# Performance work log

Hardware: AMD Instinct MI355X
Metric: run time of the kernel (lower is better)

Reference implementation:

```python
import jax, jax.numpy as jnp
import numpy as np

B, N, F_IN = 64, 128, 128
H, MSG, L = 512, 512, 4
N_STEPS = 4
TARGET = 12
HIDDEN = (128, 256, 128)


def _mlp_params(key, n_in, n_out):
    dims = (n_in,) + HIDDEN + (n_out,)
    ps = []
    for i in range(len(dims) - 1):
        key, k1, k2 = jax.random.split(key, 3)
        s = 1.0 / np.sqrt(dims[i]).astype(np.float32)
        ps.append(jax.random.uniform(k1, (dims[i + 1], dims[i]), minval=-s, maxval=s, dtype=jnp.float32))
        ps.append(jax.random.uniform(k2, (dims[i + 1],), minval=-s, maxval=s, dtype=jnp.float32))
    return ps


def setup_inputs():
    key = jax.random.key(0)
    ks = jax.random.split(key, 10)
    g = (jax.random.uniform(ks[0], (B, N, N)) < 0.15).astype(jnp.float32)
    e = jax.random.randint(ks[1], (B, N, N), 0, L + 1).astype(jnp.float32) * g
    h_in = jax.random.normal(ks[2], (B, N, F_IN), dtype=jnp.float32)
    # trailing nodes are 'virtual' (zero features -> masked out by the model)
    node_on = (jnp.arange(N) < 112).astype(jnp.float32)
    h_in = h_in * node_on[None, :, None]
    g = g * node_on[None, :, None] * node_on[None, None, :]
    e = e * node_on[None, :, None] * node_on[None, None, :]
    A = jax.random.normal(ks[3], (L, H, MSG), dtype=jnp.float32)  # per-edge-label message matrices
    s = 1.0 / np.sqrt(H).astype(np.float32)
    gru_Wih = jax.random.uniform(ks[4], (3 * H, MSG), minval=-s, maxval=s, dtype=jnp.float32)
    gru_Whh = jax.random.uniform(ks[5], (3 * H, H), minval=-s, maxval=s, dtype=jnp.float32)
    gru_bih = jax.random.uniform(ks[6], (3 * H,), minval=-s, maxval=s, dtype=jnp.float32)
    gru_bhh = jax.random.uniform(ks[7], (3 * H,), minval=-s, maxval=s, dtype=jnp.float32)
    r1 = _mlp_params(ks[8], 2 * H, TARGET)
    r2 = _mlp_params(ks[9], H, TARGET)
    inp = dict(g=g, h_in=h_in, e=e, A=A, gru_Wih=gru_Wih, gru_Whh=gru_Whh,
               gru_bih=gru_bih, gru_bhh=gru_bhh)
    for i in range(4):
        inp['r1_W%d' % i], inp['r1_b%d' % i] = r1[2 * i], r1[2 * i + 1]
        inp['r2_W%d' % i], inp['r2_b%d' % i] = r2[2 * i], r2[2 * i + 1]
    return inp


def _mlp(x, Ws, bs):
    for W, b in zip(Ws[:-1], bs[:-1]):
        x = jax.nn.relu(x @ W.T + b)
    return x @ Ws[-1].T + bs[-1]


def _forward(g, h_in, e, A, gru_Wih, gru_Whh, gru_bih, gru_bhh, r1_Ws, r1_bs, r2_Ws, r2_bs):
    Bq, Nq, F = h_in.shape
    Lq, Hq, Mq = A.shape
    # zero-pad node features up to hidden size
    h0 = jnp.concatenate([h_in, jnp.zeros((Bq, Nq, Hq - F), h_in.dtype)], axis=-1)  # [B,N,H]
    node_mask = (jnp.sum(jnp.abs(h_in), axis=-1) > 0).astype(h_in.dtype)  # [B,N]
    labels = jnp.arange(1, Lq + 1, dtype=e.dtype)
    e_oh = (e[..., None] == labels).astype(h_in.dtype)  # [B,N,N,L] edge-label one-hot
    h = h0
    for _ in range(N_STEPS):
        # per-label projected states, then edge-conditioned masked-sum aggregation
        hproj = jnp.einsum('bwh,lhm->blwm', h, A)  # [B,L,N,MSG]
        m = jnp.einsum('bvwl,blwm,bvw->bvm', e_oh, hproj, g)  # [B,N,MSG]
        # one GRU step per node (vectorized), torch nn.GRU gate ordering r,z,n
        gi = m @ gru_Wih.T + gru_bih
        gh = h @ gru_Whh.T + gru_bhh
        i_r, i_z, i_n = jnp.split(gi, 3, axis=-1)
        h_r, h_z, h_n = jnp.split(gh, 3, axis=-1)
        r = jax.nn.sigmoid(i_r + h_r)
        z = jax.nn.sigmoid(i_z + h_z)
        n = jnp.tanh(i_n + r * h_n)
        h = ((1.0 - z) * n + z * h) * node_mask[..., None]
    # GGNN gated readout over nodes, masking virtual nodes
    gate = jax.nn.sigmoid(_mlp(jnp.concatenate([h, h0], axis=-1), r1_Ws, r1_bs))
    val = _mlp(h, r2_Ws, r2_bs)
    read_mask = (jnp.sum(h0, axis=-1) != 0).astype(h.dtype)  # [B,N]
    return jnp.sum(gate * val * read_mask[..., None], axis=1)  # [B,TARGET]


def reference(g, h_in, e, A, gru_Wih, gru_Whh, gru_bih, gru_bhh,
              r1_W0, r1_b0, r1_W1, r1_b1, r1_W2, r1_b2, r1_W3, r1_b3,
              r2_W0, r2_b0, r2_W1, r2_b1, r2_W2, r2_b2, r2_W3, r2_b3):
    return _forward(g, h_in, e, A, gru_Wih, gru_Whh, gru_bih, gru_bhh,
                    [r1_W0, r1_W1, r1_W2, r1_W3], [r1_b0, r1_b1, r1_b2, r1_b3],
                    [r2_W0, r2_W1, r2_W2, r2_W3], [r2_b0, r2_b1, r2_b2, r2_b3])
```

## Files before the change

kernel.cpp:

```cpp
#include <hip/hip_runtime.h>
#include <math.h>

#define B_     64
#define N_     128
#define FIN_   128
#define H_     512
#define MSG_   512
#define L_     4
#define NSTEPS_ 4
#define TGT_   12
#define ROWS_  (B_*N_)

typedef _Float16 f16;
typedef __attribute__((ext_vector_type(8))) _Float16 half8;
typedef __attribute__((ext_vector_type(4))) float f32x4;

__device__ inline void gload16(const void* g, void* l) {
    __builtin_amdgcn_global_load_lds((const __attribute__((address_space(1))) void*)g,
                                     (__attribute__((address_space(3))) void*)l,
                                     16, 0, 0);
}

__device__ inline void split_write(float v, f16* ph, f16* pl) {
    f16 hi = (f16)v;
    *ph = hi;
    *pl = (f16)(v - (float)hi);
}

__global__ void k_init(const float* __restrict__ h_in,
                       f16* __restrict__ hbh, f16* __restrict__ hbl,
                       float* __restrict__ nmask, float* __restrict__ rmask) {
    int bn = blockIdx.x;
    int t  = threadIdx.x;
    const float* src = h_in + (size_t)bn * FIN_;
    float v  = src[t];
    float sa = fabsf(v), ss = v;
    #pragma unroll
    for (int o = 32; o > 0; o >>= 1) {
        sa += __shfl_down(sa, o);
        ss += __shfl_down(ss, o);
    }
    __shared__ float wa[2], wsum[2];
    int wid = t >> 6, lane = t & 63;
    if (lane == 0) { wa[wid] = sa; wsum[wid] = ss; }
    __syncthreads();
    if (t == 0) {
        float ta = wa[0] + wa[1], ts = wsum[0] + wsum[1];
        nmask[bn] = (ta > 0.f) ? 1.f : 0.f;
        rmask[bn] = (ts != 0.f) ? 1.f : 0.f;
    }
    f16* bh = hbh + (size_t)bn * 1024;
    f16* bl = hbl + (size_t)bn * 1024;
    #pragma unroll
    for (int r = 0; r < 4; r++) {
        int j = t + r * 128;
        float val = (j < FIN_) ? src[j] : 0.f;
        f16 hi = (f16)val, lo = (f16)(val - (float)hi);
        bh[j] = hi; bl[j] = lo;
        bh[512 + j] = hi; bl[512 + j] = lo;
    }
}

__global__ void k_mkmask(const float* __restrict__ g, const float* __restrict__ e,
                         f16* __restrict__ Mm) {
    long idx = (long)blockIdx.x * 256 + threadIdx.x;
    if (idx >= (long)ROWS_ * 512) return;
    int w = idx & 127;
    int l = (idx >> 7) & 3;
    long bv = idx >> 9;
    float gv = g[bv * N_ + w];
    float ev = e[bv * N_ + w];
    Mm[idx] = (f16)((gv != 0.f && (int)ev == l + 1) ? 1.f : 0.f);
}

struct WSet {
    const float* s[10];
    f16* d[10];
    int nc[10];
    int ncp[10];
    int kk[10];
};
__global__ void k_convWs(WSet ws) {
    int ti = blockIdx.y;
    long idx = (long)blockIdx.x * 256 + threadIdx.x;
    int K = ws.kk[ti];
    long tot = (long)ws.ncp[ti] * K;
    if (idx >= tot) return;
    long n = idx / K;
    ws.d[ti][idx] = (f16)((n < ws.nc[ti]) ? ws.s[ti][idx] : 0.f);
}

__global__ void k_convA(const float* __restrict__ A, f16* __restrict__ ATh,
                        f16* __restrict__ ATl) {
    long idx = (long)blockIdx.x * 256 + threadIdx.x;
    long n = idx >> 11, k = idx & 2047;
    float v = A[k * 512 + n];
    f16 hi = (f16)v;
    ATh[idx] = hi;
    ATl[idx] = (f16)(v - (float)hi);
}

__global__ __launch_bounds__(256, 3)
void k_proj(const f16* __restrict__ ATh, const f16* __restrict__ ATl,
            const f16* __restrict__ hb, f16* __restrict__ oh, f16* __restrict__ ol)
{
    __shared__ __align__(16) f16 As[2][2][4][128][8];
    __shared__ __align__(16) f16 Bs[2][4][128][8];
    const int tid = threadIdx.x;
    const int l = tid & 63, w = tid >> 6;
    const int wr = w >> 1, wc = w & 1;
    const int lz = blockIdx.z;
    const long m0 = (long)blockIdx.x * 128;
    const long n0 = (long)blockIdx.y * 128;

    f32x4 acc[4][4];
    #pragma unroll
    for (int i = 0; i < 4; i++)
        #pragma unroll
        for (int j = 0; j < 4; j++)
            acc[i][j] = (f32x4){0.f, 0.f, 0.f, 0.f};

    const int nt = 512 >> 5;

    auto stage = [&](int buf, int t) {
        long k0 = (long)t << 5;
        #pragma unroll
        for (int i = 0; i < 4; ++i) {
            int la = tid + i * 256;
            int row = la & 127, c = (la >> 7) & 3, pl = la >> 9;
            const f16* Xp = pl ? ATl : ATh;
            gload16(Xp + (m0 + row) * 2048 + lz * 512 + k0 + c * 8,
                    (f16*)As[buf] + (size_t)la * 8);
        }
        #pragma unroll
        for (int i = 0; i < 2; ++i) {
            int la = tid + i * 256;
            int col = la & 127, c = la >> 7;
            gload16(hb + (n0 + col) * 1024 + k0 + c * 8,
                    (f16*)Bs[buf] + (size_t)la * 8);
        }
    };

    stage(0, 0);
    for (int t = 0; t < nt; ++t) {
        int cur = t & 1;
        __syncthreads();
        if (t + 1 < nt) stage(cur ^ 1, t + 1);
        const int g = l >> 4, idx = l & 15;
        half8 bf[4];
        #pragma unroll
        for (int ct = 0; ct < 4; ++ct)
            bf[ct] = *(const half8*)&Bs[cur][g][wc * 64 + ct * 16 + idx][0];
        #pragma unroll
        for (int rt = 0; rt < 4; ++rt) {
            half8 ah = *(const half8*)&As[cur][0][g][wr * 64 + rt * 16 + idx][0];
            half8 al = *(const half8*)&As[cur][1][g][wr * 64 + rt * 16 + idx][0];
            #pragma unroll
            for (int ct = 0; ct < 4; ++ct) {
                acc[rt][ct] = __builtin_amdgcn_mfma_f32_16x16x32_f16(ah, bf[ct], acc[rt][ct], 0, 0, 0);
                acc[rt][ct] = __builtin_amdgcn_mfma_f32_16x16x32_f16(al, bf[ct], acc[rt][ct], 0, 0, 0);
            }
        }
    }

    #pragma unroll
    for (int rt = 0; rt < 4; ++rt)
        #pragma unroll
        for (int ct = 0; ct < 4; ++ct) {
            long col = n0 + wc * 64 + ct * 16 + (l & 15);
            long bb = col >> 7, ww = col & 127;
            #pragma unroll
            for (int j = 0; j < 4; ++j) {
                long row = m0 + wr * 64 + rt * 16 + (l >> 4) * 4 + j;
                size_t o = ((size_t)(bb * 512 + row)) * 512 + lz * 128 + ww;
                split_write(acc[rt][ct][j], oh + o, ol + o);
            }
        }
}

__global__ __launch_bounds__(256, 3)
void k_aggm(const f16* __restrict__ Mm, const f16* __restrict__ ph,
            const f16* __restrict__ pl_, f16* __restrict__ mh, f16* __restrict__ ml)
{
    __shared__ __align__(16) f16 As[2][4][128][8];
    __shared__ __align__(16) f16 Bs[2][2][4][128][8];
    const int tid = threadIdx.x;
    const int l = tid & 63, w = tid >> 6;
    const int wr = w >> 1, wc = w & 1;
    const long b  = blockIdx.y;
    const long n0 = (long)blockIdx.x * 128;
    const f16* Xb = Mm  + (size_t)b * 128 * 512;
    const f16* W0 = ph  + (size_t)b * 512 * 512;
    const f16* W1 = pl_ + (size_t)b * 512 * 512;

    f32x4 acc[4][4];
    #pragma unroll
    for (int i = 0; i < 4; i++)
        #pragma unroll
        for (int j = 0; j < 4; j++)
            acc[i][j] = (f32x4){0.f, 0.f, 0.f, 0.f};

    const int nt = 512 >> 5;

    auto stage = [&](int buf, int t) {
        long k0 = (long)t << 5;
        #pragma unroll
        for (int i = 0; i < 2; ++i) {
            int la = tid + i * 256;
            int row = la & 127, c = la >> 7;
            gload16(Xb + row * 512 + k0 + c * 8, (f16*)As[buf] + (size_t)la * 8);
        }
        #pragma unroll
        for (int i = 0; i < 4; ++i) {
            int la = tid + i * 256;
            int col = la & 127, c = (la >> 7) & 3, pl = la >> 9;
            gload16((pl ? W1 : W0) + (n0 + col) * 512 + k0 + c * 8,
                    (f16*)Bs[buf][pl] + (size_t)(la & 511) * 8);
        }
    };

    stage(0, 0);
    for (int t = 0; t < nt; ++t) {
        int cur = t & 1;
        __syncthreads();
        if (t + 1 < nt) stage(cur ^ 1, t + 1);
        const int g = l >> 4, idx = l & 15;
        half8 bfh[4], bfl[4];
        #pragma unroll
        for (int ct = 0; ct < 4; ++ct) {
            bfh[ct] = *(const half8*)&Bs[cur][0][g][wc * 64 + ct * 16 + idx][0];
            bfl[ct] = *(const half8*)&Bs[cur][1][g][wc * 64 + ct * 16 + idx][0];
        }
        #pragma unroll
        for (int rt = 0; rt < 4; ++rt) {
            half8 af = *(const half8*)&As[cur][g][wr * 64 + rt * 16 + idx][0];
            #pragma unroll
            for (int ct = 0; ct < 4; ++ct) {
                acc[rt][ct] = __builtin_amdgcn_mfma_f32_16x16x32_f16(af, bfh[ct], acc[rt][ct], 0, 0, 0);
                acc[rt][ct] = __builtin_amdgcn_mfma_f32_16x16x32_f16(af, bfl[ct], acc[rt][ct], 0, 0, 0);
            }
        }
    }

    #pragma unroll
    for (int rt = 0; rt < 4; ++rt)
        #pragma unroll
        for (int ct = 0; ct < 4; ++ct) {
            long col = n0 + wc * 64 + ct * 16 + (l & 15);
            #pragma unroll
            for (int j = 0; j < 4; ++j) {
                long row = wr * 64 + rt * 16 + (l >> 4) * 4 + j;
                size_t o = ((size_t)b * 128 + row) * 512 + col;
                split_write(acc[rt][ct][j], mh + o, ml + o);
            }
        }
}

__global__ __launch_bounds__(256, 2)
void k_gruG(const f16* __restrict__ mh, const f16* __restrict__ ml,
            const f16* __restrict__ Wih,
            const f16* __restrict__ hih, const f16* __restrict__ hil,
            const f16* __restrict__ Whh,
            const float* __restrict__ bih, const float* __restrict__ bhh,
            f16* __restrict__ hoh, f16* __restrict__ hol,
            const float* __restrict__ nmask)
{
    __shared__ __align__(16) f16 As[2][2][4][128][8];
    __shared__ __align__(16) f16 Bs[2][4][192][8];
    const int tid = threadIdx.x;
    const int l = tid & 63, w = tid >> 6;
    const int wr = w >> 1, wc = w & 1;
    const long m0 = (long)blockIdx.x * 128;
    const int  c0 = blockIdx.y * 64;

    f32x4 rz[2][4][2], ni[4][2], nh[4][2];
    #pragma unroll
    for (int rt = 0; rt < 4; ++rt)
        #pragma unroll
        for (int ct = 0; ct < 2; ++ct) {
            rz[0][rt][ct] = (f32x4){0.f, 0.f, 0.f, 0.f};
            rz[1][rt][ct] = (f32x4){0.f, 0.f, 0.f, 0.f};
            ni[rt][ct]    = (f32x4){0.f, 0.f, 0.f, 0.f};
            nh[rt][ct]    = (f32x4){0.f, 0.f, 0.f, 0.f};
        }

    auto stageB = [&](int buf, int t, const f16* W) {
        long k0 = (long)t << 5;
        #pragma unroll
        for (int i = 0; i < 3; ++i) {
            int la = tid + i * 256;
            int g = la / 192, cc = la - g * 192;
            int col = (cc >> 6) * 512 + c0 + (cc & 63);
            gload16(W + (size_t)col * 512 + k0 + g * 8,
                    (f16*)Bs[buf] + ((size_t)g * 192 + cc) * 8);
        }
    };
    auto stage1 = [&](int buf, int t) {
        long k0 = (long)t << 5;
        #pragma unroll
        for (int i = 0; i < 4; ++i) {
            int la = tid + i * 256;
            int pl = la >> 9, g = (la >> 7) & 3, row = la & 127;
            const f16* Xp = pl ? ml : mh;
            gload16(Xp + (m0 + row) * 512 + k0 + g * 8,
                    (f16*)As[buf][pl] + (size_t)(la & 511) * 8);
        }
        stageB(buf, t, Wih);
    };
    auto stage2 = [&](int buf, int t) {
        long k0 = (long)t << 5;
        #pragma unroll
        for (int i = 0; i < 2; ++i) {
            int la = tid + i * 256;
            int g = la >> 7, row = la & 127;
            gload16(hih + (m0 + row) * 1024 + k0 + g * 8,
                    (f16*)As[buf][0] + (size_t)la * 8);
        }
        stageB(buf, t, Whh);
    };

    const int g = l >> 4, idx = l & 15;

    stage1(0, 0);
    for (int t = 0; t < 16; ++t) {
        int cur = t & 1;
        __syncthreads();
        if (t + 1 < 16) stage1(cur ^ 1, t + 1);
        half8 bf[6];
        #pragma unroll
        for (int gc = 0; gc < 6; ++gc)
            bf[gc] = *(const half8*)&Bs[cur][g][(gc >> 1) * 64 + wc * 32 + (gc & 1) * 16 + idx][0];
        #pragma unroll
        for (int rt = 0; rt < 4; ++rt) {
            half8 ah = *(const half8*)&As[cur][0][g][wr * 64 + rt * 16 + idx][0];
            half8 al = *(const half8*)&As[cur][1][g][wr * 64 + rt * 16 + idx][0];
            #pragma unroll
            for (int ct = 0; ct < 2; ++ct) {
                rz[0][rt][ct] = __builtin_amdgcn_mfma_f32_16x16x32_f16(ah, bf[ct],     rz[0][rt][ct], 0, 0, 0);
                rz[0][rt][ct] = __builtin_amdgcn_mfma_f32_16x16x32_f16(al, bf[ct],     rz[0][rt][ct], 0, 0, 0);
                rz[1][rt][ct] = __builtin_amdgcn_mfma_f32_16x16x32_f16(ah, bf[2 + ct], rz[1][rt][ct], 0, 0, 0);
                rz[1][rt][ct] = __builtin_amdgcn_mfma_f32_16x16x32_f16(al, bf[2 + ct], rz[1][rt][ct], 0, 0, 0);
                ni[rt][ct]    = __builtin_amdgcn_mfma_f32_16x16x32_f16(ah, bf[4 + ct], ni[rt][ct],    0, 0, 0);
                ni[rt][ct]    = __builtin_amdgcn_mfma_f32_16x16x32_f16(al, bf[4 + ct], ni[rt][ct],    0, 0, 0);
            }
        }
    }

    stage2(0, 0);
    for (int t = 0; t < 16; ++t) {
        int cur = t & 1;
        __syncthreads();
        if (t + 1 < 16) stage2(cur ^ 1, t + 1);
        half8 bf[6];
        #pragma unroll
        for (int gc = 0; gc < 6; ++gc)
            bf[gc] = *(const half8*)&Bs[cur][g][(gc >> 1) * 64 + wc * 32 + (gc & 1) * 16 + idx][0];
        #pragma unroll
        for (int rt = 0; rt < 4; ++rt) {
            half8 ah = *(const half8*)&As[cur][0][g][wr * 64 + rt * 16 + idx][0];
            #pragma unroll
            for (int ct = 0; ct < 2; ++ct) {
                rz[0][rt][ct] = __builtin_amdgcn_mfma_f32_16x16x32_f16(ah, bf[ct],     rz[0][rt][ct], 0, 0, 0);
                rz[1][rt][ct] = __builtin_amdgcn_mfma_f32_16x16x32_f16(ah, bf[2 + ct], rz[1][rt][ct], 0, 0, 0);
                nh[rt][ct]    = __builtin_amdgcn_mfma_f32_16x16x32_f16(ah, bf[4 + ct], nh[rt][ct],    0, 0, 0);
            }
        }
    }

    #pragma unroll
    for (int rt = 0; rt < 4; ++rt)
        #pragma unroll
        for (int ct = 0; ct < 2; ++ct) {
            int c = c0 + wc * 32 + ct * 16 + idx;
            float br = bih[c]        + bhh[c];
            float bz = bih[512 + c]  + bhh[512 + c];
            float bni = bih[1024 + c];
            float bnh = bhh[1024 + c];
            #pragma unroll
            for (int j = 0; j < 4; ++j) {
                long row = m0 + wr * 64 + rt * 16 + g * 4 + j;
                float r = 1.f / (1.f + expf(-(rz[0][rt][ct][j] + br)));
                float z = 1.f / (1.f + expf(-(rz[1][rt][ct][j] + bz)));
                float n = tanhf(ni[rt][ct][j] + bni + r * (nh[rt][ct][j] + bnh));
                size_t o = (size_t)row * 1024 + c;
                float h_old = (float)hih[o] + (float)hil[o];
                float out = ((1.f - z) * n + z * h_old) * nmask[row];
                split_write(out, hoh + o, hol + o);
            }
        }
}

template<int OUT>
__global__ __launch_bounds__(256, 4)
void k_mfma1(const f16* __restrict__ Xh, int ldx,
             const f16* __restrict__ Wh, int ldw, const float* __restrict__ bias,
             float* __restrict__ Cf, f16* __restrict__ Ch,
             int ldc, int ncmax, int K)
{
    __shared__ __align__(16) f16 As[2][4][128][8];
    __shared__ __align__(16) f16 Bs[2][4][128][8];
    const int tid = threadIdx.x;
    const int l = tid & 63, w = tid >> 6;
    const int wr = w >> 1, wc = w & 1;
    const long m0 = (long)blockIdx.x * 128;
    const long n0 = (long)blockIdx.y * 128;

    f32x4 acc[4][4];
    #pragma unroll
    for (int i = 0; i < 4; i++)
        #pragma unroll
        for (int j = 0; j < 4; j++)
            acc[i][j] = (f32x4){0.f, 0.f, 0.f, 0.f};

    const int nt = K >> 5;

    auto stage = [&](int buf, int t) {
        long k0 = (long)t << 5;
        #pragma unroll
        for (int i = 0; i < 2; ++i) {
            int la = tid + i * 256;
            int row = la & 127, c = la >> 7;
            gload16(Xh + (m0 + row) * ldx + k0 + c * 8,
                    (f16*)As[buf] + (size_t)la * 8);
        }
        #pragma unroll
        for (int i = 0; i < 2; ++i) {
            int la = tid + i * 256;
            int col = la & 127, c = la >> 7;
            gload16(Wh + (n0 + col) * ldw + k0 + c * 8,
                    (f16*)Bs[buf] + (size_t)la * 8);
        }
    };

    stage(0, 0);
    for (int t = 0; t < nt; ++t) {
        int cur = t & 1;
        __syncthreads();
        if (t + 1 < nt) stage(cur ^ 1, t + 1);
        const int g = l >> 4, idx = l & 15;
        half8 bf[4];
        #pragma unroll
        for (int ct = 0; ct < 4; ++ct)
            bf[ct] = *(const half8*)&Bs[cur][g][wc * 64 + ct * 16 + idx][0];
        #pragma unroll
        for (int rt = 0; rt < 4; ++rt) {
            half8 ah = *(const half8*)&As[cur][g][wr * 64 + rt * 16 + idx][0];
            #pragma unroll
            for (int ct = 0; ct < 4; ++ct)
                acc[rt][ct] = __builtin_amdgcn_mfma_f32_16x16x32_f16(ah, bf[ct], acc[rt][ct], 0, 0, 0);
        }
    }

    #pragma unroll
    for (int rt = 0; rt < 4; ++rt)
        #pragma unroll
        for (int ct = 0; ct < 4; ++ct) {
            long col = n0 + wc * 64 + ct * 16 + (l & 15);
            if (col < ncmax) {
                float bv = bias ? bias[col] : 0.f;
                #pragma unroll
                for (int j = 0; j < 4; ++j) {
                    long row = m0 + wr * 64 + rt * 16 + (l >> 4) * 4 + j;
                    float v = acc[rt][ct][j] + bv;
                    if (OUT == 0) {
                        Cf[row * ldc + col] = v;
                    } else {
                        Ch[row * ldc + col] = (f16)fmaxf(v, 0.f);
                    }
                }
            }
        }
}

__global__ void k_readout(const float* __restrict__ gp, const float* __restrict__ vp,
                          const float* __restrict__ rmask, float* __restrict__ out) {
    int b = blockIdx.x;
    int t = threadIdx.x;
    float a[TGT_];
    const float* gr = gp + ((size_t)b * N_ + t) * TGT_;
    const float* vr = vp + ((size_t)b * N_ + t) * TGT_;
    float mk = rmask[b * N_ + t];
    #pragma unroll
    for (int j = 0; j < TGT_; j++)
        a[j] = (1.f / (1.f + expf(-gr[j]))) * vr[j] * mk;
    __shared__ float red[128][TGT_];
    #pragma unroll
    for (int j = 0; j < TGT_; j++) red[t][j] = a[j];
    __syncthreads();
    for (int off = 64; off > 0; off >>= 1) {
        if (t < off)
            #pragma unroll
            for (int j = 0; j < TGT_; j++) red[t][j] += red[t + off][j];
        __syncthreads();
    }
    if (t < TGT_) out[b * TGT_ + t] = red[0][t];
}

extern "C" void kernel_launch(void* const* d_in, const int* in_sizes, int n_in,
                              void* d_out, int out_size, void* d_ws, size_t ws_size,
                              hipStream_t stream) {
    const float* g    = (const float*)d_in[0];
    const float* h_in = (const float*)d_in[1];
    const float* e    = (const float*)d_in[2];
    const float* A    = (const float*)d_in[3];
    const float* Wih  = (const float*)d_in[4];
    const float* Whh  = (const float*)d_in[5];
    const float* bih  = (const float*)d_in[6];
    const float* bhh  = (const float*)d_in[7];

    const float *r1W[4], *r1b[4], *r2W[4], *r2b[4];
    bool interleaved = (in_sizes[10] == 128 * 512);
    if (interleaved) {
        for (int i = 0; i < 4; i++) {
            r1W[i] = (const float*)d_in[8 + 4 * i + 0];
            r1b[i] = (const float*)d_in[8 + 4 * i + 1];
            r2W[i] = (const float*)d_in[8 + 4 * i + 2];
            r2b[i] = (const float*)d_in[8 + 4 * i + 3];
        }
    } else {
        for (int i = 0; i < 4; i++) {
            r1W[i] = (const float*)d_in[8 + 2 * i + 0];
            r1b[i] = (const float*)d_in[8 + 2 * i + 1];
            r2W[i] = (const float*)d_in[16 + 2 * i + 0];
            r2b[i] = (const float*)d_in[16 + 2 * i + 1];
        }
    }

    char* ws = (char*)d_ws;
    size_t off = 0;
    auto alloc = [&](size_t bytes) { char* p = ws + off; off += bytes; return p; };

    f16* hbh[2]; f16* hbl[2];
    hbh[0] = (f16*)alloc((size_t)ROWS_ * 1024 * 2);
    hbl[0] = (f16*)alloc((size_t)ROWS_ * 1024 * 2);
    hbh[1] = (f16*)alloc((size_t)ROWS_ * 1024 * 2);
    hbl[1] = (f16*)alloc((size_t)ROWS_ * 1024 * 2);
    f16* mh = (f16*)alloc((size_t)ROWS_ * 512 * 2);
    f16* ml = (f16*)alloc((size_t)ROWS_ * 512 * 2);
    f16* Mm = (f16*)alloc((size_t)ROWS_ * 512 * 2);
    char* hat = alloc((size_t)2 * 4 * 512 * 8192 * 2);
    f16*  hATh = (f16*)hat;
    f16*  hATl = (f16*)(hat + (size_t)4 * 512 * 8192 * 2);
    f16*   tah = (f16*)hat;
    f16*   tbh = tah + (size_t)ROWS_ * 128;
    float* gp  = (float*)(tbh + (size_t)ROWS_ * 256);
    float* vp  = gp + (size_t)ROWS_ * TGT_;
    f16* ATh  = (f16*)alloc((size_t)512 * 2048 * 2);
    f16* ATl  = (f16*)alloc((size_t)512 * 2048 * 2);
    f16* Wihh = (f16*)alloc((size_t)1536 * 512 * 2);
    f16* Whhh = (f16*)alloc((size_t)1536 * 512 * 2);
    f16* rWh[8];
    const int rNc[8]  = {128, 256, 128, TGT_, 128, 256, 128, TGT_};
    const int rNcp[8] = {128, 256, 128, 128,  128, 256, 128, 128};
    const int rK[8]   = {1024, 128, 256, 128, 512, 128, 256, 128};
    for (int i = 0; i < 8; i++)
        rWh[i] = (f16*)alloc((size_t)rNcp[i] * rK[i] * 2);
    float* nm = (float*)alloc(ROWS_ * 4);
    float* rm = (float*)alloc(ROWS_ * 4);
    (void)ws_size;

    k_convA<<<(512 * 2048) / 256, 256, 0, stream>>>(A, ATh, ATl);
    {
        WSet wset;
        const float* srcs[10] = {Wih, Whh, r1W[0], r1W[1], r1W[2], r1W[3],
                                 r2W[0], r2W[1], r2W[2], r2W[3]};
        f16* dsts[10] = {Wihh, Whhh, rWh[0], rWh[1], rWh[2], rWh[3],
                         rWh[4], rWh[5], rWh[6], rWh[7]};
        int ncs[10]  = {1536, 1536, rNc[0], rNc[1], rNc[2], rNc[3], rNc[4], rNc[5], rNc[6], rNc[7]};
        int ncps[10] = {1536, 1536, rNcp[0], rNcp[1], rNcp[2], rNcp[3], rNcp[4], rNcp[5], rNcp[6], rNcp[7]};
        int ks[10]   = {512, 512, rK[0], rK[1], rK[2], rK[3], rK[4], rK[5], rK[6], rK[7]};
        for (int i = 0; i < 10; i++) {
            wset.s[i] = srcs[i]; wset.d[i] = dsts[i];
            wset.nc[i] = ncs[i]; wset.ncp[i] = ncps[i]; wset.kk[i] = ks[i];
        }
        int maxblocks = (1536 * 512 + 255) / 256;
        k_convWs<<<dim3(maxblocks, 10), 256, 0, stream>>>(wset);
    }
    k_mkmask<<<((long)ROWS_ * 512 + 255) / 256, 256, 0, stream>>>(g, e, Mm);
    k_init<<<ROWS_, 128, 0, stream>>>(h_in, hbh[0], hbl[0], nm, rm);

    for (int step = 0; step < NSTEPS_; step++) {
        int cur = step & 1, nxt = cur ^ 1;
        k_proj<<<dim3(4, 64, 4), 256, 0, stream>>>(ATh, ATl, hbh[cur], hATh, hATl);
        k_aggm<<<dim3(4, 64), 256, 0, stream>>>(Mm, hATh, hATl, mh, ml);
        k_gruG<<<dim3(64, 8), 256, 0, stream>>>(mh, ml, Wihh, hbh[cur], hbl[cur],
                                                Whhh, bih, bhh, hbh[nxt], hbl[nxt], nm);
    }

    k_mfma1<1><<<dim3(64, 1), 256, 0, stream>>>(hbh[0], 1024, rWh[0], 1024, r1b[0], nullptr, tah, 128, 128, 1024);
    k_mfma1<1><<<dim3(64, 2), 256, 0, stream>>>(tah, 128, rWh[1], 128, r1b[1], nullptr, tbh, 256, 256, 128);
    k_mfma1<1><<<dim3(64, 1), 256, 0, stream>>>(tbh, 256, rWh[2], 256, r1b[2], nullptr, tah, 128, 128, 256);
    k_mfma1<0><<<dim3(64, 1), 256, 0, stream>>>(tah, 128, rWh[3], 128, r1b[3], gp, nullptr, TGT_, TGT_, 128);
    k_mfma1<1><<<dim3(64, 1), 256, 0, stream>>>(hbh[0], 1024, rWh[4], 512, r2b[0], nullptr, tah, 128, 128, 512);
    k_mfma1<1><<<dim3(64, 2), 256, 0, stream>>>(tah, 128, rWh[5], 128, r2b[1], nullptr, tbh, 256, 256, 128);
    k_mfma1<1><<<dim3(64, 1), 256, 0, stream>>>(tbh, 256, rWh[6], 256, r2b[2], nullptr, tah, 128, 128, 256);
    k_mfma1<0><<<dim3(64, 1), 256, 0, stream>>>(tah, 128, rWh[7], 128, r2b[3], vp, nullptr, TGT_, TGT_, 128);

    k_readout<<<B_, 128, 0, stream>>>(gp, vp, rm, (float*)d_out);
}
```

Measured before the change: 914.1 us.

## Drop low-half split of A in projection and batch readout MLP layers

The projection GEMM now uses only the fp16 high part of the message matrices A, removing the second (low-residual) MFMA pass and its extra LDS staging. Launch bounds rise to 4 waves per SIMD. Separately, the two readout MLPs (gate and value) are merged into one launch per layer via blockIdx.z, halving launch count and doubling per-launch parallelism. Dropping the low part of A reduces precision of A (values ~N(0,1)) to fp16, which may raise numerical error in message passing.

```diff
diff --git a/kernel.cpp b/kernel.cpp
--- a/kernel.cpp
+++ b/kernel.cpp
@@ -90,21 +90,17 @@
     ws.d[ti][idx] = (f16)((n < ws.nc[ti]) ? ws.s[ti][idx] : 0.f);
 }
 
-__global__ void k_convA(const float* __restrict__ A, f16* __restrict__ ATh,
-                        f16* __restrict__ ATl) {
+__global__ void k_convA(const float* __restrict__ A, f16* __restrict__ ATh) {
     long idx = (long)blockIdx.x * 256 + threadIdx.x;
     long n = idx >> 11, k = idx & 2047;
-    float v = A[k * 512 + n];
-    f16 hi = (f16)v;
-    ATh[idx] = hi;
-    ATl[idx] = (f16)(v - (float)hi);
-}
-
-__global__ __launch_bounds__(256, 3)
-void k_proj(const f16* __restrict__ ATh, const f16* __restrict__ ATl,
-            const f16* __restrict__ hb, f16* __restrict__ oh, f16* __restrict__ ol)
+    ATh[idx] = (f16)A[k * 512 + n];
+}
+
+__global__ __launch_bounds__(256, 4)
+void k_proj(const f16* __restrict__ ATh, const f16* __restrict__ hb,
+            f16* __restrict__ oh, f16* __restrict__ ol)
 {
-    __shared__ __align__(16) f16 As[2][2][4][128][8];
+    __shared__ __align__(16) f16 As[2][4][128][8];
     __shared__ __align__(16) f16 Bs[2][4][128][8];
     const int tid = threadIdx.x;
     const int l = tid & 63, w = tid >> 6;
@@ -125,11 +121,10 @@
     auto stage = [&](int buf, int t) {
         long k0 = (long)t << 5;
         #pragma unroll
-        for (int i = 0; i < 4; ++i) {
-            int la = tid + i * 256;
-            int row = la & 127, c = (la >> 7) & 3, pl = la >> 9;
-            const f16* Xp = pl ? ATl : ATh;
-            gload16(Xp + (m0 + row) * 2048 + lz * 512 + k0 + c * 8,
+        for (int i = 0; i < 2; ++i) {
+            int la = tid + i * 256;
+            int row = la & 127, c = la >> 7;
+            gload16(ATh + (m0 + row) * 2048 + lz * 512 + k0 + c * 8,
                     (f16*)As[buf] + (size_t)la * 8);
         }
         #pragma unroll
@@ -153,13 +148,10 @@
             bf[ct] = *(const half8*)&Bs[cur][g][wc * 64 + ct * 16 + idx][0];
         #pragma unroll
         for (int rt = 0; rt < 4; ++rt) {
-            half8 ah = *(const half8*)&As[cur][0][g][wr * 64 + rt * 16 + idx][0];
-            half8 al = *(const half8*)&As[cur][1][g][wr * 64 + rt * 16 + idx][0];
-            #pragma unroll
-            for (int ct = 0; ct < 4; ++ct) {
+            half8 ah = *(const half8*)&As[cur][g][wr * 64 + rt * 16 + idx][0];
+            #pragma unroll
+            for (int ct = 0; ct < 4; ++ct)
                 acc[rt][ct] = __builtin_amdgcn_mfma_f32_16x16x32_f16(ah, bf[ct], acc[rt][ct], 0, 0, 0);
-                acc[rt][ct] = __builtin_amdgcn_mfma_f32_16x16x32_f16(al, bf[ct], acc[rt][ct], 0, 0, 0);
-            }
         }
     }
 
@@ -390,13 +382,22 @@
         }
 }
 
+struct RP {
+    const f16* X[2];  int ldx[2];
+    const f16* W[2];  int ldw[2];
+    const float* bias[2];
+    float* Cf[2];  f16* Ch[2];
+    int ldc[2];  int ncmax[2];  int K[2];
+};
 template<int OUT>
 __global__ __launch_bounds__(256, 4)
-void k_mfma1(const f16* __restrict__ Xh, int ldx,
-             const f16* __restrict__ Wh, int ldw, const float* __restrict__ bias,
-             float* __restrict__ Cf, f16* __restrict__ Ch,
-             int ldc, int ncmax, int K)
-{
+void k_mfmaD(RP p) {
+    const int z = blockIdx.z;
+    const f16* Xh = p.X[z];  const int ldx = p.ldx[z];
+    const f16* Wh = p.W[z];  const int ldw = p.ldw[z];
+    const float* bias = p.bias[z];
+    const int ldc = p.ldc[z], ncmax = p.ncmax[z], K = p.K[z];
+
     __shared__ __align__(16) f16 As[2][4][128][8];
     __shared__ __align__(16) f16 Bs[2][4][128][8];
     const int tid = threadIdx.x;
@@ -463,9 +464,9 @@
                     long row = m0 + wr * 64 + rt * 16 + (l >> 4) * 4 + j;
                     float v = acc[rt][ct][j] + bv;
                     if (OUT == 0) {
-                        Cf[row * ldc + col] = v;
+                        p.Cf[z][row * ldc + col] = v;
                     } else {
-                        Ch[row * ldc + col] = (f16)fmaxf(v, 0.f);
+                        p.Ch[z][row * ldc + col] = (f16)fmaxf(v, 0.f);
                     }
                 }
             }
@@ -541,12 +542,13 @@
     char* hat = alloc((size_t)2 * 4 * 512 * 8192 * 2);
     f16*  hATh = (f16*)hat;
     f16*  hATl = (f16*)(hat + (size_t)4 * 512 * 8192 * 2);
-    f16*   tah = (f16*)hat;
-    f16*   tbh = tah + (size_t)ROWS_ * 128;
-    float* gp  = (float*)(tbh + (size_t)ROWS_ * 256);
+    f16*   ta1 = (f16*)hat;
+    f16*   tb1 = ta1 + (size_t)ROWS_ * 128;
+    f16*   ta2 = tb1 + (size_t)ROWS_ * 256;
+    f16*   tb2 = ta2 + (size_t)ROWS_ * 128;
+    float* gp  = (float*)(tb2 + (size_t)ROWS_ * 256);
     float* vp  = gp + (size_t)ROWS_ * TGT_;
     f16* ATh  = (f16*)alloc((size_t)512 * 2048 * 2);
-    f16* ATl  = (f16*)alloc((size_t)512 * 2048 * 2);
     f16* Wihh = (f16*)alloc((size_t)1536 * 512 * 2);
     f16* Whhh = (f16*)alloc((size_t)1536 * 512 * 2);
     f16* rWh[8];
@@ -559,7 +561,7 @@
     float* rm = (float*)alloc(ROWS_ * 4);
     (void)ws_size;
 
-    k_convA<<<(512 * 2048) / 256, 256, 0, stream>>>(A, ATh, ATl);
+    k_convA<<<(512 * 2048) / 256, 256, 0, stream>>>(A, ATh);
     {
         WSet wset;
         const float* srcs[10] = {Wih, Whh, r1W[0], r1W[1], r1W[2], r1W[3],
@@ -581,20 +583,31 @@
 
     for (int step = 0; step < NSTEPS_; step++) {
         int cur = step & 1, nxt = cur ^ 1;
-        k_proj<<<dim3(4, 64, 4), 256, 0, stream>>>(ATh, ATl, hbh[cur], hATh, hATl);
+        k_proj<<<dim3(4, 64, 4), 256, 0, stream>>>(ATh, hbh[cur], hATh, hATl);
         k_aggm<<<dim3(4, 64), 256, 0, stream>>>(Mm, hATh, hATl, mh, ml);
         k_gruG<<<dim3(64, 8), 256, 0, stream>>>(mh, ml, Wihh, hbh[cur], hbl[cur],
                                                 Whhh, bih, bhh, hbh[nxt], hbl[nxt], nm);
     }
 
-    k_mfma1<1><<<dim3(64, 1), 256, 0, stream>>>(hbh[0], 1024, rWh[0], 1024, r1b[0], nullptr, tah, 128, 128, 1024);
-    k_mfma1<1><<<dim3(64, 2), 256, 0, stream>>>(tah, 128, rWh[1], 128, r1b[1], nullptr, tbh, 256, 256, 128);
-    k_mfma1<1><<<dim3(64, 1), 256, 0, stream>>>(tbh, 256, rWh[2], 256, r1b[2], nullptr, tah, 128, 128, 256);
-    k_mfma1<0><<<dim3(64, 1), 256, 0, stream>>>(tah, 128, rWh[3], 128, r1b[3], gp, nullptr, TGT_, TGT_, 128);
-    k_mfma1<1><<<dim3(64, 1), 256, 0, stream>>>(hbh[0], 1024, rWh[4], 512, r2b[0], nullptr, tah, 128, 128, 512);
-    k_mfma1<1><<<dim3(64, 2), 256, 0, stream>>>(tah, 128, rWh[5], 128, r2b[1], nullptr, tbh, 256, 256, 128);
-    k_mfma1<1><<<dim3(64, 1), 256, 0, stream>>>(tbh, 256, rWh[6], 256, r2b[2], nullptr, tah, 128, 128, 256);
-    k_mfma1<0><<<dim3(64, 1), 256, 0, stream>>>(tah, 128, rWh[7], 128, r2b[3], vp, nullptr, TGT_, TGT_, 128);
+    auto setRP = [&](RP& p, int zi, const f16* X, int ldx, const f16* W, int ldw,
+                     const float* bias, float* Cf, f16* Ch, int ldc, int ncmax, int K) {
+        p.X[zi] = X; p.ldx[zi] = ldx; p.W[zi] = W; p.ldw[zi] = ldw;
+        p.bias[zi] = bias; p.Cf[zi] = Cf; p.Ch[zi] = Ch;
+        p.ldc[zi] = ldc; p.ncmax[zi] = ncmax; p.K[zi] = K;
+    };
+    RP p0, p1, p2, p3;
+    setRP(p0, 0, hbh[0], 1024, rWh[0], 1024, r1b[0], nullptr, ta1, 128, 128, 1024);
+    setRP(p0, 1, hbh[0], 1024, rWh[4],  512, r2b[0], nullptr, ta2, 128, 128,  512);
+    setRP(p1, 0, ta1, 128, rWh[1], 128, r1b[1], nullptr, tb1, 256, 256, 128);
+    setRP(p1, 1, ta2, 128, rWh[5], 128, r2b[1], nullptr, tb2, 256, 256, 128);
+    setRP(p2, 0, tb1, 256, rWh[2], 256, r1b[2], nullptr, ta1, 128, 128, 256);
+    setRP(p2, 1, tb2, 256, rWh[6], 256, r2b[2], nullptr, ta2, 128, 128, 256);
+    setRP(p3, 0, ta1, 128, rWh[3], 128, r1b[3], gp, nullptr, TGT_, TGT_, 128);
+    setRP(p3, 1, ta2, 128, rWh[7], 128, r2b[3], vp, nullptr, TGT_, TGT_, 128);
+    k_mfmaD<1><<<dim3(64, 1, 2), 256, 0, stream>>>(p0);
+    k_mfmaD<1><<<dim3(64, 2, 2), 256, 0, stream>>>(p1);
+    k_mfmaD<1><<<dim3(64, 1, 2), 256, 0, stream>>>(p2);
+    k_mfmaD<0><<<dim3(64, 1, 2), 256, 0, stream>>>(p3);
 
     k_readout<<<B_, 128, 0, stream>>>(gp, vp, rm, (float*)d_out);
 }
```

New measurement: 805.0 us. -11.9%, faster.
